# Performance work log

Hardware: AMD Instinct MI355X
Metric: run time of the kernel (lower is better)

Reference implementation:

```python
import jax, jax.numpy as jnp
import numpy as np

DIM = 1024
C = 128
B = 8
T = 2048


def setup_inputs() -> dict:
    key = jax.random.key(0)
    ks = jax.random.split(key, 16)
    s = 0.02
    inp = {
        "x": jax.random.normal(ks[0], (B, T, DIM), dtype=jnp.float32),
        "Wq": jax.random.normal(ks[1], (DIM, C), dtype=jnp.float32) * s,
        "bq": jnp.zeros((C,), dtype=jnp.float32),
        "Wk": jax.random.normal(ks[2], (DIM, C), dtype=jnp.float32) * s,
        "bk": jnp.zeros((C,), dtype=jnp.float32),
        "Wv": jax.random.normal(ks[3], (DIM, C), dtype=jnp.float32) * s,
        "bv": jnp.zeros((C,), dtype=jnp.float32),
        "Wa": jax.random.normal(ks[4], (DIM, 1), dtype=jnp.float32) * s,
        "ba": jnp.zeros((1,), dtype=jnp.float32),
        "Wb": jax.random.normal(ks[5], (DIM, 1), dtype=jnp.float32) * s,
        "bb": jnp.zeros((1,), dtype=jnp.float32),
        "Wg": jax.random.normal(ks[6], (DIM, C), dtype=jnp.float32) * s,
        "bg": jnp.zeros((C,), dtype=jnp.float32),
        "Wo": jax.random.normal(ks[7], (C, DIM), dtype=jnp.float32) * s,
        "bo": jnp.zeros((DIM,), dtype=jnp.float32),
    }
    return inp


def reference(x, Wq, bq, Wk, bk, Wv, bv, Wa, ba, Wb, bb, Wg, bg, Wo, bo):
    # projections
    q = x @ Wq + bq                                   # [B,T,C]
    kr = x @ Wk + bk
    k = kr / jnp.maximum(jnp.linalg.norm(kr, axis=-1, keepdims=True), 1e-12)  # F.normalize
    v = x @ Wv + bv
    alpha = jax.nn.sigmoid(x @ Wa + ba)               # [B,T,1]
    beta = jax.nn.sigmoid(x @ Wb + bb)                # [B,T,1]
    gate = jax.nn.sigmoid(x @ Wg + bg)                # [B,T,C]

    def step(S, inp):
        q_t, k_t, v_t, a_t, b_t, g_t = inp            # [B,C],[B,C],[B,C],[B,1],[B,1],[B,C]
        # S @ (a*(I - b k k^T)) = a*(S - b*(S k) k^T)  (rank-1 form, no CxC bmm)
        Sk = jnp.einsum('bij,bj->bi', S, k_t)         # [B,C]
        a = a_t[:, :, None]                            # [B,1,1]
        b = b_t[:, :, None]
        S_new = a * (S - b * (Sk[:, :, None] * k_t[:, None, :])) \
                + b * (v_t[:, :, None] * k_t[:, None, :])
        o = jnp.einsum('bi,bij->bj', q_t, S_new) * g_t  # [B,C]
        return S_new, o

    seq = (
        jnp.swapaxes(q, 0, 1), jnp.swapaxes(k, 0, 1), jnp.swapaxes(v, 0, 1),
        jnp.swapaxes(alpha, 0, 1), jnp.swapaxes(beta, 0, 1), jnp.swapaxes(gate, 0, 1),
    )
    S0 = jnp.zeros((x.shape[0], C, C), dtype=x.dtype)
    _, outs = jax.lax.scan(step, S0, seq)             # [T,B,C]
    o = jnp.swapaxes(outs, 0, 1)                      # [B,T,C]
    return o @ Wo + bo                                # [B,T,DIM]
```

## Files before the change

kernel.cpp:

```cpp
#include <hip/hip_runtime.h>
#include <hip/hip_fp16.h>
#include <cstdint>

#define MB 8
#define TT 2048
#define DIMK 1024
#define CC 128
#define NG 32
#define MROWS (MB*TT)
#define NPROJ 576
#define YSTR 576

using bf16x8 = __attribute__((__ext_vector_type__(8))) __bf16;
using f32x4v = __attribute__((__ext_vector_type__(4))) float;
using f32x2v = __attribute__((__ext_vector_type__(2))) float;

__device__ __forceinline__ unsigned short f2b(float f) {
    unsigned u = __float_as_uint(f);
    u += 0x7fffu + ((u >> 16) & 1u);
    return (unsigned short)(u >> 16);
}

__global__ __launch_bounds__(256) void cast_x_kernel(
    const float* __restrict__ in, unsigned short* __restrict__ outp)
{
    size_t i = ((size_t)blockIdx.x * 256 + threadIdx.x) * 8;
    float4 a = *(const float4*)(in + i);
    float4 b = *(const float4*)(in + i + 4);
    uint4 r;
    r.x = f2b(a.x) | ((unsigned)f2b(a.y) << 16);
    r.y = f2b(a.z) | ((unsigned)f2b(a.w) << 16);
    r.z = f2b(b.x) | ((unsigned)f2b(b.y) << 16);
    r.w = f2b(b.z) | ((unsigned)f2b(b.w) << 16);
    *(uint4*)(outp + i) = r;
}

__global__ __launch_bounds__(256) void pack_wt(
    const float* __restrict__ Wq, const float* __restrict__ Wk,
    const float* __restrict__ Wv, const float* __restrict__ Wg,
    const float* __restrict__ Wa, const float* __restrict__ Wb,
    unsigned short* __restrict__ WcatT)
{
    int idx = blockIdx.x * 256 + threadIdx.x;
    if (idx >= NPROJ * DIMK) return;
    int n = idx >> 10, k = idx & 1023;
    float v = 0.f;
    if      (n < 128) v = Wq[k * 128 + n];
    else if (n < 256) v = Wk[k * 128 + (n - 128)];
    else if (n < 384) v = Wv[k * 128 + (n - 256)];
    else if (n < 512) v = Wg[k * 128 + (n - 384)];
    else if (n == 512) v = Wa[k];
    else if (n == 513) v = Wb[k];
    WcatT[idx] = f2b(v);
}

__global__ void pack_bias(const float* __restrict__ bq, const float* __restrict__ bk,
                          const float* __restrict__ bv, const float* __restrict__ bg,
                          const float* __restrict__ ba, const float* __restrict__ bb,
                          float* __restrict__ biascat)
{
    int n = threadIdx.x;
    if (n >= NPROJ) return;
    float v = 0.f;
    if      (n < 128) v = bq[n];
    else if (n < 256) v = bk[n - 128];
    else if (n < 384) v = bv[n - 256];
    else if (n < 512) v = bg[n - 384];
    else if (n == 512) v = ba[0];
    else if (n == 513) v = bb[0];
    biascat[n] = v;
}

__global__ __launch_bounds__(256) void cast_wot(
    const float* __restrict__ Wo, unsigned short* __restrict__ WoT)
{
    int idx = blockIdx.x * 256 + threadIdx.x;
    if (idx >= DIMK * CC) return;
    int n = idx >> 7, k = idx & 127;
    WoT[idx] = f2b(Wo[k * DIMK + n]);
}

__global__ __launch_bounds__(256) void gemm_bt_bf16(
    const unsigned short* __restrict__ A, const unsigned short* __restrict__ BT,
    const float* __restrict__ bias, float* __restrict__ C,
    int M, int N, int K)
{
    __shared__ unsigned short As[4][128][8];
    __shared__ unsigned short Bs[4][64][8];
    int tid = threadIdx.x;
    int w = tid >> 6, l = tid & 63;
    int lm = l & 15, lq = l >> 4;
    int bm = blockIdx.y * 128, bn = blockIdx.x * 64;

    f32x4v acc[2][4];
#pragma unroll
    for (int rt = 0; rt < 2; rt++)
#pragma unroll
        for (int ct = 0; ct < 4; ct++) acc[rt][ct] = (f32x4v)(0.f);

    int ar = tid >> 1, ah = tid & 1;
    int brn = tid >> 2, bq = tid & 3;
    const unsigned short* Arow = A + (size_t)(bm + ar) * K + ah * 16;
    const unsigned short* Brow = BT + (size_t)(bn + brn) * K + bq * 8;

    for (int kk = 0; kk < K; kk += 32) {
        uint4 av0 = *(const uint4*)(Arow + kk);
        uint4 av1 = *(const uint4*)(Arow + kk + 8);
        uint4 bv  = *(const uint4*)(Brow + kk);
        __syncthreads();
        *(uint4*)&As[ah * 2][ar][0]     = av0;
        *(uint4*)&As[ah * 2 + 1][ar][0] = av1;
        *(uint4*)&Bs[bq][brn][0]        = bv;
        __syncthreads();
        bf16x8 af[2], bf[4];
#pragma unroll
        for (int rt = 0; rt < 2; rt++)
            __builtin_memcpy(&af[rt], &As[lq][w * 32 + rt * 16 + lm][0], 16);
#pragma unroll
        for (int ct = 0; ct < 4; ct++)
            __builtin_memcpy(&bf[ct], &Bs[lq][ct * 16 + lm][0], 16);
#pragma unroll
        for (int rt = 0; rt < 2; rt++)
#pragma unroll
            for (int ct = 0; ct < 4; ct++)
                acc[rt][ct] = __builtin_amdgcn_mfma_f32_16x16x32_bf16(
                    af[rt], bf[ct], acc[rt][ct], 0, 0, 0);
    }
#pragma unroll
    for (int rt = 0; rt < 2; rt++)
#pragma unroll
        for (int ct = 0; ct < 4; ct++) {
            int col = bn + ct * 16 + lm;
            float bcol = bias[col];
#pragma unroll
            for (int i = 0; i < 4; i++) {
                int row = bm + w * 32 + rt * 16 + lq * 4 + i;
                C[(size_t)row * N + col] = acc[rt][ct][i] + bcol;
            }
        }
}

__global__ __launch_bounds__(64) void postproj_kernel(
    const float* __restrict__ Y, float* __restrict__ knorm,
    float* __restrict__ gbuf, float4* __restrict__ qvab)
{
    int m = blockIdx.x;
    int lane = threadIdx.x;
    int b = m >> 11, t = m & (TT - 1);
    const float* yr = Y + (size_t)m * YSTR;
    float k0 = yr[128 + lane], k1 = yr[192 + lane];
    float ss = k0 * k0 + k1 * k1;
#pragma unroll
    for (int mask = 1; mask < 64; mask <<= 1) ss += __shfl_xor(ss, mask);
    float inv = 1.0f / fmaxf(sqrtf(ss), 1e-12f);
    knorm[(size_t)m * CC + lane]      = k0 * inv;
    knorm[(size_t)m * CC + 64 + lane] = k1 * inv;
    float g0 = yr[384 + lane], g1 = yr[448 + lane];
    gbuf[(size_t)m * CC + lane]      = 1.f / (1.f + expf(-g0));
    gbuf[(size_t)m * CC + 64 + lane] = 1.f / (1.f + expf(-g1));
    float a  = 1.f / (1.f + expf(-yr[512]));
    float bb = 1.f / (1.f + expf(-yr[513]));
    {
        int i = lane;
        qvab[((size_t)(b * NG + (i >> 2)) * TT + t) * 4 + (i & 3)] =
            make_float4(yr[i], yr[256 + i], a, bb);
        i = lane + 64;
        qvab[((size_t)(b * NG + (i >> 2)) * TT + t) * 4 + (i & 3)] =
            make_float4(yr[i], yr[256 + i], a, bb);
    }
}

__device__ __forceinline__ float dpp_add_xor1(float p) {
    int i = __builtin_amdgcn_mov_dpp(__float_as_int(p), 0xB1, 0xF, 0xF, true);
    return p + __int_as_float(i);
}
__device__ __forceinline__ float dpp_add_xor2(float p) {
    int i = __builtin_amdgcn_mov_dpp(__float_as_int(p), 0x4E, 0xF, 0xF, true);
    return p + __int_as_float(i);
}
__device__ __forceinline__ float dpp_add_mirror7(float p) {
    int i = __builtin_amdgcn_mov_dpp(__float_as_int(p), 0x141, 0xF, 0xF, true);
    return p + __int_as_float(i);
}
__device__ __forceinline__ float dpp_add_ror8(float p) {
    int i = __builtin_amdgcn_mov_dpp(__float_as_int(p), 0x128, 0xF, 0xF, true);
    return p + __int_as_float(i);
}
__device__ __forceinline__ int h2i(__half2 h) { int i; __builtin_memcpy(&i, &h, 4); return i; }
__device__ __forceinline__ __half2 i2h(int i) { __half2 h; __builtin_memcpy(&h, &i, 4); return h; }

__device__ __forceinline__ f32x2v vfma2(f32x2v a, f32x2v b, f32x2v c) {
#if __has_builtin(__builtin_elementwise_fma)
    return __builtin_elementwise_fma(a, b, c);
#else
    return a * b + c;
#endif
}
__device__ __forceinline__ __half2 cvt2h(f32x2v v) {
    return __float22half2_rn(make_float2(v.x, v.y));
}

__device__ __forceinline__ void pl16_swap(unsigned &a, unsigned &b) {
#if __has_builtin(__builtin_amdgcn_permlane16_swap)
    auto r = __builtin_amdgcn_permlane16_swap(a, b, false, false);
    a = (unsigned)r[0]; b = (unsigned)r[1];
#else
    asm volatile("v_permlane16_swap_b32 %0, %1" : "+v"(a), "+v"(b));
#endif
}
__device__ __forceinline__ void pl32_swap(unsigned &a, unsigned &b) {
#if __has_builtin(__builtin_amdgcn_permlane32_swap)
    auto r = __builtin_amdgcn_permlane32_swap(a, b, false, false);
    a = (unsigned)r[0]; b = (unsigned)r[1];
#else
    asm volatile("v_permlane32_swap_b32 %0, %1" : "+v"(a), "+v"(b));
#endif
}
__device__ __forceinline__ float pl16_add(float p) {
    unsigned a = __float_as_uint(p), b = a;
    pl16_swap(a, b);
    return __uint_as_float(a) + __uint_as_float(b);
}
__device__ __forceinline__ float pl32_add(float p) {
    unsigned a = __float_as_uint(p), b = a;
    pl32_swap(a, b);
    return __uint_as_float(a) + __uint_as_float(b);
}

__device__ __forceinline__ void gload_lds16(const void* g, void* l) {
    __builtin_amdgcn_global_load_lds(
        (const __attribute__((address_space(1))) void*)g,
        (__attribute__((address_space(3))) void*)l, 16, 0, 0);
}

#define CH  32
#define NCH (TT/CH)

template <bool ATOMIC>
__global__ __launch_bounds__(256, 1) void scan_kernel(
    const float* __restrict__ knorm, const float4* __restrict__ qvab,
    void* __restrict__ outp)
{
    __shared__ float lk[2 * CH * 128];
    __shared__ float lq[2 * CH * 16];
    __shared__ unsigned outb[2 * 4 * CH * 64];

    int blk = blockIdx.x;
    int b = blk >> 5;
    int gi = blk & 31;
    int tid = threadIdx.x;
    int w = tid >> 6, lane = tid & 63;
    f32x2v s2v = (f32x2v)(0.f);
    size_t mbase = (size_t)b * TT;

    const char* kgb = (const char*)(knorm + mbase * CC);
    const char* qgb = (const char*)(qvab + (size_t)blk * TT * 4);
    size_t lane16 = (size_t)lane * 16;

#define STAGE_CHUNK(cc, bf) do {                                              \
    char* lkd = (char*)lk + (size_t)(bf) * (CH * 512) + (size_t)w * 4096;     \
    const char* kc_ = kgb + (size_t)(cc) * (CH * 512) + (size_t)w * 4096;     \
    _Pragma("unroll")                                                         \
    for (int i_ = 0; i_ < 4; ++i_)                                            \
        gload_lds16(kc_ + (size_t)i_ * 1024 + lane16, lkd + i_ * 1024);       \
    if (w == 0) {                                                             \
        char* lqd = (char*)lq + (size_t)(bf) * (CH * 64);                     \
        const char* qc_ = qgb + (size_t)(cc) * (CH * 64);                     \
        gload_lds16(qc_ + lane16, lqd);                                       \
        gload_lds16(qc_ + 1024 + lane16, lqd + 1024);                         \
    }                                                                         \
} while (0)

#define LDK(st, sl) do {                                                      \
    kP[sl] = *(const f32x2v*)(lkc + (st) * 128 + lane * 2);                   \
    qP[sl] = *(const f32x4v*)(lqc + (st) * 16 + w * 4);                       \
} while (0)

#define KSTEP(st, sl) do {                                                    \
    f32x2v k2 = kP[sl];                                                       \
    f32x4v qv = qP[sl];                                                       \
    float q_ = qv[0], v_ = qv[1], at_ = qv[2], bt_ = qv[3];                   \
    f32x2v ps_ = s2v * k2;                                                    \
    float p_ = ps_[0] + ps_[1];                                               \
    p_ = dpp_add_xor1(p_);                                                    \
    p_ = dpp_add_xor2(p_);                                                    \
    p_ = dpp_add_mirror7(p_);                                                 \
    p_ = dpp_add_ror8(p_);                                                    \
    p_ = pl16_add(p_);                                                        \
    p_ = pl32_add(p_);                                                        \
    float ba_ = at_ * bt_, bv_ = bt_ * v_;                                    \
    float cr_ = fmaf(-ba_, p_, bv_);                                          \
    f32x2v at2_ = {at_, at_};                                                 \
    f32x2v cr2_ = {cr_, cr_};                                                 \
    f32x2v q2_  = {q_, q_};                                                   \
    s2v = vfma2(k2, cr2_, s2v * at2_);                                        \
    __half2 pb_ = cvt2h(q2_ * s2v);                                           \
    obw[(st) * 64] = (unsigned)h2i(pb_);                                      \
} while (0)

#define COMBINE(cc) do {                                                      \
    const unsigned* ob_ = outb + (size_t)((cc) & 1) * (4 * CH * 64);          \
    int tg_ = (cc) * CH;                                                      \
    _Pragma("unroll")                                                         \
    for (int j_ = 0; j_ < 8; ++j_) {                                          \
        int slot_ = tid + 256 * j_;                                           \
        int st_ = slot_ >> 6, ln_ = slot_ & 63;                               \
        __half2 h0_ = i2h((int)ob_[(0 * CH + st_) * 64 + ln_]);               \
        __half2 h1_ = i2h((int)ob_[(1 * CH + st_) * 64 + ln_]);               \
        __half2 h2_ = i2h((int)ob_[(2 * CH + st_) * 64 + ln_]);               \
        __half2 h3_ = i2h((int)ob_[(3 * CH + st_) * 64 + ln_]);               \
        __half2 r_ = __hadd2(__hadd2(h0_, h1_), __hadd2(h2_, h3_));           \
        size_t m_ = mbase + tg_ + st_;                                        \
        if (ATOMIC) {                                                         \
            float2 f_ = __half22float2(r_);                                   \
            float* op_ = (float*)outp + m_ * CC + ln_ * 2;                    \
            atomicAdd(op_, f_.x);                                             \
            atomicAdd(op_ + 1, f_.y);                                         \
        } else {                                                              \
            ((unsigned*)outp)[((size_t)gi * MROWS + m_) * 64 + ln_] =         \
                (unsigned)h2i(r_);                                            \
        }                                                                     \
    }                                                                         \
} while (0)

    STAGE_CHUNK(0, 0);

    for (int c = 0; c < NCH; ++c) {
        int cur = c & 1;
        if (c + 1 < NCH) STAGE_CHUNK(c + 1, cur ^ 1);
        if (c < 2) {
            asm volatile("s_waitcnt vmcnt(4)" ::: "memory");
        } else if (c + 1 < NCH) {
            asm volatile("s_waitcnt vmcnt(12)" ::: "memory");
        } else {
            asm volatile("s_waitcnt vmcnt(8)" ::: "memory");
        }
        asm volatile("s_waitcnt lgkmcnt(0)" ::: "memory");
        __builtin_amdgcn_s_barrier();
        if (c > 0) COMBINE(c - 1);

        const float* lkc = lk + (size_t)cur * CH * 128;
        const float* lqc = lq + (size_t)cur * CH * 16;
        unsigned* obw = outb + (size_t)(cur * 4 + w) * CH * 64 + lane;

        f32x2v kP[4];
        f32x4v qP[4];
        LDK(0, 0); LDK(1, 1); LDK(2, 2);
#pragma unroll
        for (int st = 0; st < CH; ++st) {
            if (st + 3 < CH) LDK(st + 3, (st + 3) & 3);
            KSTEP(st, st & 3);
        }
    }
    asm volatile("s_waitcnt lgkmcnt(0)" ::: "memory");
    __builtin_amdgcn_s_barrier();
    COMBINE(NCH - 1);
#undef STAGE_CHUNK
#undef LDK
#undef KSTEP
#undef COMBINE
}

__global__ __launch_bounds__(256) void combine_kernel(
    const unsigned* __restrict__ opart,
    const float* __restrict__ gbuf, unsigned* __restrict__ ocombb)
{
    size_t idx = (size_t)blockIdx.x * 256 + threadIdx.x;
    float sx = 0.f, sy = 0.f;
#pragma unroll
    for (int gi = 0; gi < NG; ++gi) {
        __half2 h = i2h((int)opart[(size_t)gi * MROWS * 64 + idx]);
        float2 f = __half22float2(h);
        sx += f.x; sy += f.y;
    }
    float2 g = *(const float2*)(gbuf + idx * 2);
    ocombb[idx] = f2b(sx * g.x) | ((unsigned)f2b(sy * g.y) << 16);
}

__global__ __launch_bounds__(256) void gate_kernel(
    const float* __restrict__ ocombf, const float* __restrict__ gbuf,
    unsigned short* __restrict__ ocombb)
{
    size_t idx = (size_t)blockIdx.x * 256 + threadIdx.x;
    ocombb[idx] = f2b(ocombf[idx] * gbuf[idx]);
}

extern "C" void kernel_launch(void* const* d_in, const int* in_sizes, int n_in,
                              void* d_out, int out_size, void* d_ws, size_t ws_size,
                              hipStream_t stream)
{
    const float* x  = (const float*)d_in[0];
    const float* Wq = (const float*)d_in[1];
    const float* bq = (const float*)d_in[2];
    const float* Wk = (const float*)d_in[3];
    const float* bk = (const float*)d_in[4];
    const float* Wv = (const float*)d_in[5];
    const float* bv = (const float*)d_in[6];
    const float* Wa = (const float*)d_in[7];
    const float* ba = (const float*)d_in[8];
    const float* Wb = (const float*)d_in[9];
    const float* bb = (const float*)d_in[10];
    const float* Wg = (const float*)d_in[11];
    const float* bg = (const float*)d_in[12];
    const float* Wo = (const float*)d_in[13];
    const float* bo = (const float*)d_in[14];
    float* out = (float*)d_out;

    float* ws = (float*)d_ws;
    size_t off = 0;
    float* knorm   = ws + off; off += (size_t)MROWS * CC;
    float* gbuf    = ws + off; off += (size_t)MROWS * CC;
    unsigned* ocombb = (unsigned*)(ws + off); off += (size_t)MROWS * CC / 2;
    unsigned short* WcatT = (unsigned short*)(ws + off); off += (size_t)NPROJ * DIMK / 2;
    unsigned short* WoT   = (unsigned short*)(ws + off); off += (size_t)DIMK * CC / 2;
    float* biascat = ws + off; off += NPROJ;
    unsigned short* xb = (unsigned short*)(ws + off);
    float* qvab    = ws + off; off += (size_t)MROWS * DIMK / 2;
    float* Y       = ws + off;
    size_t opart_off = off;
    off += (size_t)MROWS * YSTR;
    float* ocombf  = ws + opart_off;
    unsigned* opart = (unsigned*)(ws + opart_off);
    size_t opart_end = opart_off + (size_t)NG * MROWS * 64;
    size_t need_big = (opart_end > off ? opart_end : off) * sizeof(float);
    bool big = ws_size >= need_big;

    hipLaunchKernelGGL(cast_x_kernel, dim3((size_t)MROWS * DIMK / 8 / 256), dim3(256), 0, stream,
                       x, xb);
    hipLaunchKernelGGL(pack_wt, dim3(NPROJ * DIMK / 256), dim3(256), 0, stream,
                       Wq, Wk, Wv, Wg, Wa, Wb, WcatT);
    hipLaunchKernelGGL(pack_bias, dim3(1), dim3(NPROJ), 0, stream,
                       bq, bk, bv, bg, ba, bb, biascat);
    hipLaunchKernelGGL(cast_wot, dim3(DIMK * CC / 256), dim3(256), 0, stream,
                       Wo, WoT);
    hipLaunchKernelGGL(gemm_bt_bf16, dim3(NPROJ / 64, MROWS / 128), dim3(256), 0, stream,
                       xb, WcatT, biascat, Y, MROWS, NPROJ, DIMK);
    hipLaunchKernelGGL(postproj_kernel, dim3(MROWS), dim3(64), 0, stream,
                       Y, knorm, gbuf, (float4*)qvab);
    if (big) {
        hipLaunchKernelGGL((scan_kernel<false>), dim3(MB * NG), dim3(256), 0, stream,
                           knorm, (const float4*)qvab, (void*)opart);
        hipLaunchKernelGGL(combine_kernel, dim3(MROWS * 64 / 256), dim3(256), 0, stream,
                           opart, gbuf, ocombb);
    } else {
        (void)hipMemsetAsync(ocombf, 0, (size_t)MROWS * CC * sizeof(float), stream);
        hipLaunchKernelGGL((scan_kernel<true>), dim3(MB * NG), dim3(256), 0, stream,
                           knorm, (const float4*)qvab, (void*)ocombf);
        hipLaunchKernelGGL(gate_kernel, dim3(MROWS * CC / 256), dim3(256), 0, stream,
                           ocombf, gbuf, (unsigned short*)ocombb);
    }
    hipLaunchKernelGGL(gemm_bt_bf16, dim3(DIMK / 64, MROWS / 128), dim3(256), 0, stream,
                       (const unsigned short*)ocombb, WoT, bo, out, MROWS, DIMK, CC);
}
```

Before: 440.0 us.

## Pack two state rows per wave in scan kernel, halving threads per block

The scan kernel now runs 128 threads per block instead of 256. Each wave holds two state rows split across half-waves, and each lane keeps four columns of state instead of two. This removes the cross-32 permlane reduction step and halves the wave count per recurrence. In exchange, each lane does twice as much serial FMA work per step, and the staging and wait counts are retuned for the larger per-wave loads.

Result: slower. 467.4 us (+6.2%).

```diff
diff --git a/kernel.cpp b/kernel.cpp
--- a/kernel.cpp
+++ b/kernel.cpp
@@ -19,6 +19,12 @@
     unsigned u = __float_as_uint(f);
     u += 0x7fffu + ((u >> 16) & 1u);
     return (unsigned short)(u >> 16);
+}
+
+__device__ __forceinline__ void gload_lds16(const void* g, void* l) {
+    __builtin_amdgcn_global_load_lds(
+        (const __attribute__((address_space(1))) void*)g,
+        (__attribute__((address_space(3))) void*)l, 16, 0, 0);
 }
 
 __global__ __launch_bounds__(256) void cast_x_kernel(
@@ -208,36 +214,17 @@
     asm volatile("v_permlane16_swap_b32 %0, %1" : "+v"(a), "+v"(b));
 #endif
 }
-__device__ __forceinline__ void pl32_swap(unsigned &a, unsigned &b) {
-#if __has_builtin(__builtin_amdgcn_permlane32_swap)
-    auto r = __builtin_amdgcn_permlane32_swap(a, b, false, false);
-    a = (unsigned)r[0]; b = (unsigned)r[1];
-#else
-    asm volatile("v_permlane32_swap_b32 %0, %1" : "+v"(a), "+v"(b));
-#endif
-}
 __device__ __forceinline__ float pl16_add(float p) {
     unsigned a = __float_as_uint(p), b = a;
     pl16_swap(a, b);
     return __uint_as_float(a) + __uint_as_float(b);
 }
-__device__ __forceinline__ float pl32_add(float p) {
-    unsigned a = __float_as_uint(p), b = a;
-    pl32_swap(a, b);
-    return __uint_as_float(a) + __uint_as_float(b);
-}
-
-__device__ __forceinline__ void gload_lds16(const void* g, void* l) {
-    __builtin_amdgcn_global_load_lds(
-        (const __attribute__((address_space(1))) void*)g,
-        (__attribute__((address_space(3))) void*)l, 16, 0, 0);
-}
 
 #define CH  32
 #define NCH (TT/CH)
 
 template <bool ATOMIC>
-__global__ __launch_bounds__(256, 1) void scan_kernel(
+__global__ __launch_bounds__(128, 1) void scan_kernel(
     const float* __restrict__ knorm, const float4* __restrict__ qvab,
     void* __restrict__ outp)
 {
@@ -250,7 +237,11 @@
     int gi = blk & 31;
     int tid = threadIdx.x;
     int w = tid >> 6, lane = tid & 63;
-    f32x2v s2v = (f32x2v)(0.f);
+    int half = lane >> 5;
+    int row = 2 * w + half;
+    int cl = lane & 31;
+    f32x2v s0 = (f32x2v)(0.f);
+    f32x2v s1 = (f32x2v)(0.f);
     size_t mbase = (size_t)b * TT;
 
     const char* kgb = (const char*)(knorm + mbase * CC);
@@ -258,52 +249,57 @@
     size_t lane16 = (size_t)lane * 16;
 
 #define STAGE_CHUNK(cc, bf) do {                                              \
-    char* lkd = (char*)lk + (size_t)(bf) * (CH * 512) + (size_t)w * 4096;     \
-    const char* kc_ = kgb + (size_t)(cc) * (CH * 512) + (size_t)w * 4096;     \
+    char* lkd = (char*)lk + (size_t)(bf) * (CH * 512) + (size_t)w * 8192;     \
+    const char* kc_ = kgb + (size_t)(cc) * (CH * 512) + (size_t)w * 8192;     \
     _Pragma("unroll")                                                         \
-    for (int i_ = 0; i_ < 4; ++i_)                                            \
+    for (int i_ = 0; i_ < 8; ++i_)                                            \
         gload_lds16(kc_ + (size_t)i_ * 1024 + lane16, lkd + i_ * 1024);       \
-    if (w == 0) {                                                             \
-        char* lqd = (char*)lq + (size_t)(bf) * (CH * 64);                     \
-        const char* qc_ = qgb + (size_t)(cc) * (CH * 64);                     \
+    {                                                                         \
+        char* lqd = (char*)lq + (size_t)(bf) * (CH * 64) + (size_t)w * 1024;  \
+        const char* qc_ = qgb + (size_t)(cc) * (CH * 64) + (size_t)w * 1024;  \
         gload_lds16(qc_ + lane16, lqd);                                       \
-        gload_lds16(qc_ + 1024 + lane16, lqd + 1024);                         \
     }                                                                         \
 } while (0)
 
 #define LDK(st, sl) do {                                                      \
-    kP[sl] = *(const f32x2v*)(lkc + (st) * 128 + lane * 2);                   \
-    qP[sl] = *(const f32x4v*)(lqc + (st) * 16 + w * 4);                       \
+    kP[sl] = *(const f32x4v*)(lkc + (st) * 128 + cl * 4);                     \
+    qP[sl] = *(const f32x4v*)(lqc + (st) * 16 + row * 4);                     \
 } while (0)
 
 #define KSTEP(st, sl) do {                                                    \
-    f32x2v k2 = kP[sl];                                                       \
+    f32x4v k4 = kP[sl];                                                       \
     f32x4v qv = qP[sl];                                                       \
-    float q_ = qv[0], v_ = qv[1], at_ = qv[2], bt_ = qv[3];                   \
-    f32x2v ps_ = s2v * k2;                                                    \
-    float p_ = ps_[0] + ps_[1];                                               \
+    f32x2v k20 = __builtin_shufflevector(k4, k4, 0, 1);                       \
+    f32x2v k21 = __builtin_shufflevector(k4, k4, 2, 3);                       \
+    f32x2v ps0 = s0 * k20;                                                    \
+    f32x2v ps1 = s1 * k21;                                                    \
+    f32x2v pss = ps0 + ps1;                                                   \
+    float p_ = pss[0] + pss[1];                                               \
     p_ = dpp_add_xor1(p_);                                                    \
     p_ = dpp_add_xor2(p_);                                                    \
     p_ = dpp_add_mirror7(p_);                                                 \
-    p_ = dpp_add_ror8(p_);                                                    \
-    p_ = pl16_add(p_);                                                        \
-    p_ = pl32_add(p_);                                                        \
+    p_ = dpp_add_ror8(p_);                               \
+    p_ = pl16_add(p_);            \
+    float q_ = qv[0], v_ = qv[1], at_ = qv[2], bt_ = qv[3];                   \
     float ba_ = at_ * bt_, bv_ = bt_ * v_;                                    \
     float cr_ = fmaf(-ba_, p_, bv_);                                          \
     f32x2v at2_ = {at_, at_};                                                 \
     f32x2v cr2_ = {cr_, cr_};                                                 \
     f32x2v q2_  = {q_, q_};                                                   \
-    s2v = vfma2(k2, cr2_, s2v * at2_);                                        \
-    __half2 pb_ = cvt2h(q2_ * s2v);                                           \
-    obw[(st) * 64] = (unsigned)h2i(pb_);                                      \
+    s0 = vfma2(k20, cr2_, s0 * at2_);                                         \
+    s1 = vfma2(k21, cr2_, s1 * at2_);                                         \
+    __half2 o0_ = cvt2h(q2_ * s0);                                            \
+    __half2 o1_ = cvt2h(q2_ * s1);                                            \
+    *(uint2*)(obw + (st) * 64) =                                              \
+        make_uint2((unsigned)h2i(o0_), (unsigned)h2i(o1_));                   \
 } while (0)
 
 #define COMBINE(cc) do {                                                      \
     const unsigned* ob_ = outb + (size_t)((cc) & 1) * (4 * CH * 64);          \
     int tg_ = (cc) * CH;                                                      \
     _Pragma("unroll")                                                         \
-    for (int j_ = 0; j_ < 8; ++j_) {                                          \
-        int slot_ = tid + 256 * j_;                                           \
+    for (int j_ = 0; j_ < 16; ++j_) {                                         \
+        int slot_ = tid + 128 * j_;                                           \
         int st_ = slot_ >> 6, ln_ = slot_ & 63;                               \
         __half2 h0_ = i2h((int)ob_[(0 * CH + st_) * 64 + ln_]);               \
         __half2 h1_ = i2h((int)ob_[(1 * CH + st_) * 64 + ln_]);               \
@@ -329,11 +325,11 @@
         int cur = c & 1;
         if (c + 1 < NCH) STAGE_CHUNK(c + 1, cur ^ 1);
         if (c < 2) {
-            asm volatile("s_waitcnt vmcnt(4)" ::: "memory");
+            asm volatile("s_waitcnt vmcnt(9)" ::: "memory");
         } else if (c + 1 < NCH) {
-            asm volatile("s_waitcnt vmcnt(12)" ::: "memory");
+            asm volatile("s_waitcnt vmcnt(25)" ::: "memory");
         } else {
-            asm volatile("s_waitcnt vmcnt(8)" ::: "memory");
+            asm volatile("s_waitcnt vmcnt(16)" ::: "memory");
         }
         asm volatile("s_waitcnt lgkmcnt(0)" ::: "memory");
         __builtin_amdgcn_s_barrier();
@@ -341,9 +337,9 @@
 
         const float* lkc = lk + (size_t)cur * CH * 128;
         const float* lqc = lq + (size_t)cur * CH * 16;
-        unsigned* obw = outb + (size_t)(cur * 4 + w) * CH * 64 + lane;
-
-        f32x2v kP[4];
+        unsigned* obw = outb + (size_t)(cur * 4 + row) * CH * 64 + cl * 2;
+
+        f32x4v kP[4];
         f32x4v qP[4];
         LDK(0, 0); LDK(1, 1); LDK(2, 2);
 #pragma unroll
@@ -438,13 +434,13 @@
     hipLaunchKernelGGL(postproj_kernel, dim3(MROWS), dim3(64), 0, stream,
                        Y, knorm, gbuf, (float4*)qvab);
     if (big) {
-        hipLaunchKernelGGL((scan_kernel<false>), dim3(MB * NG), dim3(256), 0, stream,
+        hipLaunchKernelGGL((scan_kernel<false>), dim3(MB * NG), dim3(128), 0, stream,
                            knorm, (const float4*)qvab, (void*)opart);
         hipLaunchKernelGGL(combine_kernel, dim3(MROWS * 64 / 256), dim3(256), 0, stream,
                            opart, gbuf, ocombb);
     } else {
         (void)hipMemsetAsync(ocombf, 0, (size_t)MROWS * CC * sizeof(float), stream);
-        hipLaunchKernelGGL((scan_kernel<true>), dim3(MB * NG), dim3(256), 0, stream,
+        hipLaunchKernelGGL((scan_kernel<true>), dim3(MB * NG), dim3(128), 0, stream,
                            knorm, (const float4*)qvab, (void*)ocombf);
         hipLaunchKernelGGL(gate_kernel, dim3(MROWS * CC / 256), dim3(256), 0, stream,
                            ocombf, gbuf, (unsigned short*)ocombb);
```

## Precompute key Gram blocks to batch cross-lane reductions off the scan critical path

Applied to the files above, without the earlier changes.

Adds a gram_kernel that computes pairwise k_t·k_j dot products within sub-chunks of 8 timesteps. The scan then computes all 8 S·k reductions up front from the same starting state and patches them with a scalar recurrence using the Gram entries. This takes the serial wavefront-wide reduction out of each timestep's dependency chain and lets 8 reductions overlap. It costs an extra kernel launch, extra LDS staging and more registers, and the reordered arithmetic may change numerical error.

Result: slower. 493.8 us (+12.2%).

```diff
diff --git a/kernel.cpp b/kernel.cpp
--- a/kernel.cpp
+++ b/kernel.cpp
@@ -10,6 +10,7 @@
 #define MROWS (MB*TT)
 #define NPROJ 576
 #define YSTR 576
+#define RSUB 8
 
 using bf16x8 = __attribute__((__ext_vector_type__(8))) __bf16;
 using f32x4v = __attribute__((__ext_vector_type__(4))) float;
@@ -19,6 +20,12 @@
     unsigned u = __float_as_uint(f);
     u += 0x7fffu + ((u >> 16) & 1u);
     return (unsigned short)(u >> 16);
+}
+
+__device__ __forceinline__ void gload_lds16(const void* g, void* l) {
+    __builtin_amdgcn_global_load_lds(
+        (const __attribute__((address_space(1))) void*)g,
+        (__attribute__((address_space(3))) void*)l, 16, 0, 0);
 }
 
 __global__ __launch_bounds__(256) void cast_x_kernel(
@@ -226,11 +233,39 @@
     pl32_swap(a, b);
     return __uint_as_float(a) + __uint_as_float(b);
 }
-
-__device__ __forceinline__ void gload_lds16(const void* g, void* l) {
-    __builtin_amdgcn_global_load_lds(
-        (const __attribute__((address_space(1))) void*)g,
-        (__attribute__((address_space(3))) void*)l, 16, 0, 0);
+__device__ __forceinline__ float red_full(float h) {
+    h = dpp_add_xor1(h);
+    h = dpp_add_xor2(h);
+    h = dpp_add_mirror7(h);
+    h = dpp_add_ror8(h);
+    h = pl16_add(h);
+    h = pl32_add(h);
+    return h;
+}
+
+#define GIDX(t, j) ((t) * 7 - (t) * ((t) - 1) / 2 + ((j) - (t) - 1))
+
+__global__ __launch_bounds__(64) void gram_kernel(
+    const float* __restrict__ knorm, float* __restrict__ gram)
+{
+    int blk = blockIdx.x;
+    int b = blk >> 8, sc = blk & 255;
+    int lane = threadIdx.x;
+    const float* kb = knorm + ((size_t)b * TT + (size_t)sc * RSUB) * CC;
+    f32x2v k2[RSUB];
+#pragma unroll
+    for (int j = 0; j < RSUB; ++j)
+        k2[j] = *(const f32x2v*)(kb + j * CC + lane * 2);
+    float vout = 0.f;
+#pragma unroll
+    for (int t = 0; t < RSUB - 1; ++t)
+#pragma unroll
+        for (int j = t + 1; j < RSUB; ++j) {
+            f32x2v ps = k2[t] * k2[j];
+            float h = red_full(ps[0] + ps[1]);
+            vout = (lane == GIDX(t, j)) ? h : vout;
+        }
+    gram[(size_t)blk * 64 + lane] = vout;
 }
 
 #define CH  32
@@ -239,10 +274,11 @@
 template <bool ATOMIC>
 __global__ __launch_bounds__(256, 1) void scan_kernel(
     const float* __restrict__ knorm, const float4* __restrict__ qvab,
-    void* __restrict__ outp)
+    const float* __restrict__ gram, void* __restrict__ outp)
 {
     __shared__ float lk[2 * CH * 128];
     __shared__ float lq[2 * CH * 16];
+    __shared__ float lg[2 * 4 * 64];
     __shared__ unsigned outb[2 * 4 * CH * 64];
 
     int blk = blockIdx.x;
@@ -255,6 +291,7 @@
 
     const char* kgb = (const char*)(knorm + mbase * CC);
     const char* qgb = (const char*)(qvab + (size_t)blk * TT * 4);
+    const char* ggb = (const char*)(gram + (size_t)b * (TT / RSUB) * 64);
     size_t lane16 = (size_t)lane * 16;
 
 #define STAGE_CHUNK(cc, bf) do {                                              \
@@ -268,34 +305,9 @@
         const char* qc_ = qgb + (size_t)(cc) * (CH * 64);                     \
         gload_lds16(qc_ + lane16, lqd);                                       \
         gload_lds16(qc_ + 1024 + lane16, lqd + 1024);                         \
+        char* lgd = (char*)lg + (size_t)(bf) * 1024;                          \
+        gload_lds16(ggb + (size_t)(cc) * 1024 + lane16, lgd);                 \
     }                                                                         \
-} while (0)
-
-#define LDK(st, sl) do {                                                      \
-    kP[sl] = *(const f32x2v*)(lkc + (st) * 128 + lane * 2);                   \
-    qP[sl] = *(const f32x4v*)(lqc + (st) * 16 + w * 4);                       \
-} while (0)
-
-#define KSTEP(st, sl) do {                                                    \
-    f32x2v k2 = kP[sl];                                                       \
-    f32x4v qv = qP[sl];                                                       \
-    float q_ = qv[0], v_ = qv[1], at_ = qv[2], bt_ = qv[3];                   \
-    f32x2v ps_ = s2v * k2;                                                    \
-    float p_ = ps_[0] + ps_[1];                                               \
-    p_ = dpp_add_xor1(p_);                                                    \
-    p_ = dpp_add_xor2(p_);                                                    \
-    p_ = dpp_add_mirror7(p_);                                                 \
-    p_ = dpp_add_ror8(p_);                                                    \
-    p_ = pl16_add(p_);                                                        \
-    p_ = pl32_add(p_);                                                        \
-    float ba_ = at_ * bt_, bv_ = bt_ * v_;                                    \
-    float cr_ = fmaf(-ba_, p_, bv_);                                          \
-    f32x2v at2_ = {at_, at_};                                                 \
-    f32x2v cr2_ = {cr_, cr_};                                                 \
-    f32x2v q2_  = {q_, q_};                                                   \
-    s2v = vfma2(k2, cr2_, s2v * at2_);                                        \
-    __half2 pb_ = cvt2h(q2_ * s2v);                                           \
-    obw[(st) * 64] = (unsigned)h2i(pb_);                                      \
 } while (0)
 
 #define COMBINE(cc) do {                                                      \
@@ -341,23 +353,57 @@
 
         const float* lkc = lk + (size_t)cur * CH * 128;
         const float* lqc = lq + (size_t)cur * CH * 16;
+        const float* lgc0 = lg + (size_t)cur * (4 * 64);
         unsigned* obw = outb + (size_t)(cur * 4 + w) * CH * 64 + lane;
 
-        f32x2v kP[4];
-        f32x4v qP[4];
-        LDK(0, 0); LDK(1, 1); LDK(2, 2);
-#pragma unroll
-        for (int st = 0; st < CH; ++st) {
-            if (st + 3 < CH) LDK(st + 3, (st + 3) & 3);
-            KSTEP(st, st & 3);
+#pragma unroll
+        for (int r = 0; r < CH / RSUB; ++r) {
+            const float* lks = lkc + r * RSUB * 128;
+            const float* lqs = lqc + r * RSUB * 16;
+            const float* lgs = lgc0 + r * 64;
+            f32x2v k2[RSUB];
+            f32x4v qp[RSUB];
+            f32x4v g4[7];
+#pragma unroll
+            for (int j = 0; j < RSUB; ++j)
+                k2[j] = *(const f32x2v*)(lks + j * 128 + lane * 2);
+#pragma unroll
+            for (int j = 0; j < RSUB; ++j)
+                qp[j] = *(const f32x4v*)(lqs + j * 16 + w * 4);
+#pragma unroll
+            for (int j = 0; j < 7; ++j)
+                g4[j] = *(const f32x4v*)(lgs + j * 4);
+            float wv[RSUB];
+#pragma unroll
+            for (int j = 0; j < RSUB; ++j) {
+                f32x2v ps = s2v * k2[j];
+                wv[j] = red_full(ps[0] + ps[1]);
+            }
+#pragma unroll
+            for (int t = 0; t < RSUB; ++t) {
+                float p_ = wv[t];
+                float q_ = qp[t][0], v_ = qp[t][1], a_ = qp[t][2], b_ = qp[t][3];
+                float ba_ = a_ * b_, bv_ = b_ * v_;
+                float c_ = fmaf(-ba_, p_, bv_);
+                f32x2v a2_ = {a_, a_};
+                f32x2v c2_ = {c_, c_};
+                f32x2v q2_ = {q_, q_};
+                s2v = vfma2(k2[t], c2_, s2v * a2_);
+                __half2 pb_ = cvt2h(q2_ * s2v);
+                obw[(r * RSUB + t) * 64] = (unsigned)h2i(pb_);
+#pragma unroll
+                for (int j = t + 1; j < RSUB; ++j) {
+                    const int gi_ = GIDX(t, j);
+                    float g_ = g4[gi_ >> 2][gi_ & 3];
+                    wv[j] = fmaf(a_, wv[j], c_ * g_);
+                }
+            }
         }
     }
     asm volatile("s_waitcnt lgkmcnt(0)" ::: "memory");
     __builtin_amdgcn_s_barrier();
     COMBINE(NCH - 1);
 #undef STAGE_CHUNK
-#undef LDK
-#undef KSTEP
 #undef COMBINE
 }
 
@@ -414,6 +460,7 @@
     unsigned short* WcatT = (unsigned short*)(ws + off); off += (size_t)NPROJ * DIMK / 2;
     unsigned short* WoT   = (unsigned short*)(ws + off); off += (size_t)DIMK * CC / 2;
     float* biascat = ws + off; off += NPROJ;
+    float* gram    = ws + off; off += (size_t)MB * (TT / RSUB) * 64;
     unsigned short* xb = (unsigned short*)(ws + off);
     float* qvab    = ws + off; off += (size_t)MROWS * DIMK / 2;
     float* Y       = ws + off;
@@ -437,15 +484,17 @@
                        xb, WcatT, biascat, Y, MROWS, NPROJ, DIMK);
     hipLaunchKernelGGL(postproj_kernel, dim3(MROWS), dim3(64), 0, stream,
                        Y, knorm, gbuf, (float4*)qvab);
+    hipLaunchKernelGGL(gram_kernel, dim3(MB * (TT / RSUB)), dim3(64), 0, stream,
+                       knorm, gram);
     if (big) {
         hipLaunchKernelGGL((scan_kernel<false>), dim3(MB * NG), dim3(256), 0, stream,
-                           knorm, (const float4*)qvab, (void*)opart);
+                           knorm, (const float4*)qvab, gram, (void*)opart);
         hipLaunchKernelGGL(combine_kernel, dim3(MROWS * 64 / 256), dim3(256), 0, stream,
                            opart, gbuf, ocombb);
     } else {
         (void)hipMemsetAsync(ocombf, 0, (size_t)MROWS * CC * sizeof(float), stream);
         hipLaunchKernelGGL((scan_kernel<true>), dim3(MB * NG), dim3(256), 0, stream,
-                           knorm, (const float4*)qvab, (void*)ocombf);
+                           knorm, (const float4*)qvab, gram, (void*)ocombf);
         hipLaunchKernelGGL(gate_kernel, dim3(MROWS * CC / 256), dim3(256), 0, stream,
                            ocombf, gbuf, (unsigned short*)ocombb);
     }
```
